# Performance work log

Measured on AMD Instinct MI355X. Metric: run time of the kernel, lower is better.

Reference implementation:

```python
import jax, jax.numpy as jnp
import numpy as np

D = 1024
M = 256
BATCH = 2048


def setup_inputs() -> dict:
    key = jax.random.key(0)
    kx, kw, kp = jax.random.split(key, 3)
    x = jax.random.uniform(kx, (BATCH, D), dtype=jnp.float32)
    W = jax.random.normal(kw, (M,), dtype=jnp.float32)
    P = jax.random.normal(kp, (M, D), dtype=jnp.float32)
    return {"x": x, "W": W, "P": P}


def reference(x, W, P):
    # log mixture weights: log softmax over m
    logw = jax.nn.log_softmax(W, axis=-1)              # [m]
    p = jax.nn.sigmoid(P)                              # [m, d]
    # broadcast Bernoulli likelihood: [batch, m, d]
    lik = x[:, None, :] * p[None, :, :] + (1.0 - x[:, None, :]) * (1.0 - p[None, :, :])
    # per-component log-likelihood summed over features, plus log weight
    comp_ll = jnp.sum(jnp.log(lik), axis=-1) + logw[None, :]   # [batch, m]
    # mixture log-likelihood via logsumexp over components
    return jax.scipy.special.logsumexp(comp_ll, axis=-1)       # [batch]
```

## Files before the change

### kernel.cpp

```cpp
#include <hip/hip_runtime.h>

#define BATCH 2048
#define MM    256
#define DD    1024

#define BB 128
#define BM 64
#define KC 16
#define TB 8
#define TM 4
#define LXS (BB + 4)
#define LRS (BM + 4)
#define NBT (BATCH / BB)

#define LOG2E 1.4426950408889634f
#define LN2   0.6931471805599453f

typedef float v2f __attribute__((ext_vector_type(2)));

__device__ __forceinline__ float fr_mant(float x) {
#if __has_builtin(__builtin_amdgcn_frexp_mantf)
    return __builtin_amdgcn_frexp_mantf(x);
#else
    unsigned u = __float_as_uint(x);
    return __uint_as_float((u & 0x807FFFFFu) | 0x3F000000u);
#endif
}
__device__ __forceinline__ int fr_exp(float x) {
#if __has_builtin(__builtin_amdgcn_frexp_expf)
    return __builtin_amdgcn_frexp_expf(x);
#else
    return (int)((__float_as_uint(x) >> 23) & 0xFFu) - 126;
#endif
}

__global__ __launch_bounds__(256) void precomp_kernel(
        const float* __restrict__ P, const float* __restrict__ Wv,
        float* __restrict__ rbuf, float* __restrict__ cst) {
    const int m = blockIdx.x;
    const int t = threadIdx.x;
    const int lane = t & 63, wid = t >> 6;

    float4 z = ((const float4*)(P + (size_t)m * DD))[t];
    float e0 = __expf(z.x), e1 = __expf(z.y), e2 = __expf(z.z), e3 = __expf(z.w);
    ((float4*)(rbuf + (size_t)m * DD))[t] =
        make_float4(e0 - 1.f, e1 - 1.f, e2 - 1.f, e3 - 1.f);
    float part = -(__log2f(1.f + e0) + __log2f(1.f + e1) +
                   __log2f(1.f + e2) + __log2f(1.f + e3));

    __shared__ float smA[4], smB[4];

    #pragma unroll
    for (int o = 32; o; o >>= 1) part += __shfl_xor(part, o);
    if (lane == 0) smA[wid] = part;

    float w = Wv[t];
    float mx = w;
    #pragma unroll
    for (int o = 32; o; o >>= 1) mx = fmaxf(mx, __shfl_xor(mx, o));
    if (lane == 0) smB[wid] = mx;
    __syncthreads();

    float rowc = smA[0] + smA[1] + smA[2] + smA[3];
    float gmx  = fmaxf(fmaxf(smB[0], smB[1]), fmaxf(smB[2], smB[3]));

    float se = __expf(w - gmx);
    #pragma unroll
    for (int o = 32; o; o >>= 1) se += __shfl_xor(se, o);
    __syncthreads();
    if (lane == 0) smA[wid] = se;
    __syncthreads();

    if (t == 0) {
        float sum = smA[0] + smA[1] + smA[2] + smA[3];
        cst[m] = rowc + (Wv[m] - gmx) * LOG2E - __log2f(sum);
    }
}

__global__ __launch_bounds__(256, 4) void main_kernel(
        const float* __restrict__ x, const float* __restrict__ rbuf,
        float* __restrict__ pbuf, int dc) {
    __shared__ __align__(16) float lx[KC * LXS];
    __shared__ __align__(16) float lr[KC * LRS];

    const int tid = threadIdx.x;
    const int tx = tid & 15;
    const int ty = tid >> 4;

    const int gid  = blockIdx.x;
    const int xcd  = gid & 7;
    const int k    = gid >> 3;
    const int m_id = k & 3;
    const int tile = (k >> 2) * 8 + xcd;
    const int b_id = tile & (NBT - 1);
    const int d_id = tile / NBT;

    const int m0 = m_id * BM;
    const int b0 = b_id * BB;
    const int d0 = d_id * dc;
    const int NC = dc / KC;

    const int rowx = tid >> 2, segx = tid & 3;
    const float* xp0 = x + (size_t)(b0 + rowx) * DD + d0 + segx * 4;
    const float* xp1 = xp0 + (size_t)64 * DD;
    const float* rp  = rbuf + (size_t)(m0 + rowx) * DD + d0 + segx * 4;

    float4 cx0 = *(const float4*)xp0;
    float4 cx1 = *(const float4*)xp1;
    float4 cr  = *(const float4*)rp;

    v2f prod2[TB / 2][TM];
    int acce[TB][TM];
    #pragma unroll
    for (int i2 = 0; i2 < TB / 2; ++i2)
        #pragma unroll
        for (int j = 0; j < TM; ++j) prod2[i2][j] = (v2f){1.0f, 1.0f};
    #pragma unroll
    for (int i = 0; i < TB; ++i)
        #pragma unroll
        for (int j = 0; j < TM; ++j) acce[i][j] = 0;

    const v2f one2 = (v2f){1.0f, 1.0f};

    for (int c = 0; c < NC; ++c) {
        __syncthreads();
        {
            const int base = segx * 4;
            lx[(base + 0) * LXS + rowx] = cx0.x;
            lx[(base + 1) * LXS + rowx] = cx0.y;
            lx[(base + 2) * LXS + rowx] = cx0.z;
            lx[(base + 3) * LXS + rowx] = cx0.w;
            lx[(base + 0) * LXS + rowx + 64] = cx1.x;
            lx[(base + 1) * LXS + rowx + 64] = cx1.y;
            lx[(base + 2) * LXS + rowx + 64] = cx1.z;
            lx[(base + 3) * LXS + rowx + 64] = cx1.w;
            if (rowx < BM) {
                lr[(base + 0) * LRS + rowx] = cr.x;
                lr[(base + 1) * LRS + rowx] = cr.y;
                lr[(base + 2) * LRS + rowx] = cr.z;
                lr[(base + 3) * LRS + rowx] = cr.w;
            }
        }
        if (c + 1 < NC) {
            xp0 += KC; xp1 += KC; rp += KC;
            cx0 = *(const float4*)xp0;
            cx1 = *(const float4*)xp1;
            cr  = *(const float4*)rp;
        }
        __syncthreads();

        #pragma unroll
        for (int kc = 0; kc < KC; ++kc) {
            const float4* xp = (const float4*)&lx[kc * LXS + TB * ty];
            float4 xa = xp[0], xb = xp[1];
            const float4* rpf = (const float4*)&lr[kc * LRS + TM * tx];
            float4 rv = rpf[0];
            v2f xs[TB / 2] = {(v2f){xa.x, xa.y}, (v2f){xa.z, xa.w},
                              (v2f){xb.x, xb.y}, (v2f){xb.z, xb.w}};
            v2f rs[TM] = {(v2f){rv.x, rv.x}, (v2f){rv.y, rv.y},
                          (v2f){rv.z, rv.z}, (v2f){rv.w, rv.w}};
            #pragma unroll
            for (int i2 = 0; i2 < TB / 2; ++i2)
                #pragma unroll
                for (int j = 0; j < TM; ++j) {
                    v2f t = __builtin_elementwise_fma(xs[i2], rs[j], one2);
                    prod2[i2][j] = prod2[i2][j] * t;
                }
        }
        #pragma unroll
        for (int i2 = 0; i2 < TB / 2; ++i2)
            #pragma unroll
            for (int j = 0; j < TM; ++j) {
                float p0 = prod2[i2][j].x, p1 = prod2[i2][j].y;
                acce[2 * i2 + 0][j] += fr_exp(p0);
                acce[2 * i2 + 1][j] += fr_exp(p1);
                prod2[i2][j] = (v2f){fr_mant(p0), fr_mant(p1)};
            }
    }

    float* pb = pbuf + ((size_t)d_id * BATCH + b0) * MM + m0;
    #pragma unroll
    for (int i = 0; i < TB; ++i) {
        const int i2 = i >> 1;
        float p0 = (i & 1) ? prod2[i2][0].y : prod2[i2][0].x;
        float p1 = (i & 1) ? prod2[i2][1].y : prod2[i2][1].x;
        float p2 = (i & 1) ? prod2[i2][2].y : prod2[i2][2].x;
        float p3 = (i & 1) ? prod2[i2][3].y : prod2[i2][3].x;
        float4 vv;
        vv.x = (float)acce[i][0] + __log2f(p0);
        vv.y = (float)acce[i][1] + __log2f(p1);
        vv.z = (float)acce[i][2] + __log2f(p2);
        vv.w = (float)acce[i][3] + __log2f(p3);
        *(float4*)&pb[(size_t)(TB * ty + i) * MM + TM * tx] = vv;
    }
}

__global__ __launch_bounds__(256) void finalize16_kernel(
        const float4* __restrict__ pbuf4, const float4* __restrict__ cst4,
        float* __restrict__ out) {
    const int lane = threadIdx.x & 63;
    const int w = threadIdx.x >> 6;
    const int b = blockIdx.x * 4 + w;

    float4 v = cst4[lane];
    const float4* pb = pbuf4 + (size_t)b * (MM / 4) + lane;
    #pragma unroll
    for (int s = 0; s < 16; ++s) {
        float4 t = pb[(size_t)s * BATCH * (MM / 4)];
        v.x += t.x; v.y += t.y; v.z += t.z; v.w += t.w;
    }

    float mx = fmaxf(fmaxf(v.x, v.y), fmaxf(v.z, v.w));
    #pragma unroll
    for (int o = 32; o; o >>= 1) mx = fmaxf(mx, __shfl_xor(mx, o));

    float s = exp2f(v.x - mx) + exp2f(v.y - mx) + exp2f(v.z - mx) + exp2f(v.w - mx);
    #pragma unroll
    for (int o = 32; o; o >>= 1) s += __shfl_xor(s, o);

    if (lane == 0) out[b] = LN2 * (mx + __log2f(s));
}

__global__ __launch_bounds__(256) void finalize_kernel(
        const float* __restrict__ pbuf, const float* __restrict__ cst,
        float* __restrict__ out, int sd) {
    const int lane = threadIdx.x & 63;
    const int w = threadIdx.x >> 6;
    const int b = blockIdx.x * 4 + w;

    float v0 = cst[lane];
    float v1 = cst[lane + 64];
    float v2 = cst[lane + 128];
    float v3 = cst[lane + 192];

    for (int s = 0; s < sd; ++s) {
        const float* row = pbuf + ((size_t)s * BATCH + b) * MM;
        v0 += row[lane];
        v1 += row[lane + 64];
        v2 += row[lane + 128];
        v3 += row[lane + 192];
    }

    float mx = fmaxf(fmaxf(v0, v1), fmaxf(v2, v3));
    #pragma unroll
    for (int o = 32; o; o >>= 1) mx = fmaxf(mx, __shfl_xor(mx, o));

    float s = exp2f(v0 - mx) + exp2f(v1 - mx) + exp2f(v2 - mx) + exp2f(v3 - mx);
    #pragma unroll
    for (int o = 32; o; o >>= 1) s += __shfl_xor(s, o);

    if (lane == 0) out[b] = LN2 * (mx + __log2f(s));
}

extern "C" void kernel_launch(void* const* d_in, const int* in_sizes, int n_in,
                              void* d_out, int out_size, void* d_ws, size_t ws_size,
                              hipStream_t stream) {
    const float* x  = (const float*)d_in[0];
    const float* Wv = (const float*)d_in[1];
    const float* P  = (const float*)d_in[2];

    float* ws   = (float*)d_ws;
    float* rbuf = ws;
    float* cst  = rbuf + (size_t)MM * DD;
    float* pbuf = cst + MM;

    size_t fixed = ((size_t)MM * DD + MM) * sizeof(float);
    size_t avail = (ws_size > fixed) ? (ws_size - fixed) : 0;
    int sd = 16;
    while (sd > 1 && (size_t)sd * BATCH * MM * sizeof(float) > avail) sd >>= 1;

    precomp_kernel<<<MM, 256, 0, stream>>>(P, Wv, rbuf, cst);
    int nblocks = NBT * sd * 4;
    main_kernel<<<nblocks, 256, 0, stream>>>(x, rbuf, pbuf, DD / sd);
    if (sd == 16)
        finalize16_kernel<<<BATCH / 4, 256, 0, stream>>>(
            (const float4*)pbuf, (const float4*)cst, (float*)d_out);
    else
        finalize_kernel<<<BATCH / 4, 256, 0, stream>>>(pbuf, cst, (float*)d_out, sd);
}
```

Measured before the change: 93.74 us.

## Enlarge main kernel tile to 128x128 with 8x8 per-thread register blocking

Doubles the component tile (BM 64→128) and per-thread component count (TM 4→8), so each thread computes an 8x8 block of products. The global-to-LDS load mapping is reworked so each thread loads two float4 per operand, and the column split is strided at 64 to avoid bank conflicts. The goal is fewer LDS reads and fewer redundant x loads per FMA. In exchange, register pressure roughly doubles, occupancy is lowered to 2 blocks per SIMD, and the grid has half as many blocks.

```diff
diff --git a/kernel.cpp b/kernel.cpp
--- a/kernel.cpp
+++ b/kernel.cpp
@@ -5,13 +5,14 @@
 #define DD    1024
 
 #define BB 128
-#define BM 64
+#define BM 128
 #define KC 16
 #define TB 8
-#define TM 4
+#define TM 8
 #define LXS (BB + 4)
 #define LRS (BM + 4)
 #define NBT (BATCH / BB)
+#define NMB (MM / BM)
 
 #define LOG2E 1.4426950408889634f
 #define LN2   0.6931471805599453f
@@ -77,7 +78,7 @@
     }
 }
 
-__global__ __launch_bounds__(256, 4) void main_kernel(
+__global__ __launch_bounds__(256, 2) void main_kernel(
         const float* __restrict__ x, const float* __restrict__ rbuf,
         float* __restrict__ pbuf, int dc) {
     __shared__ __align__(16) float lx[KC * LXS];
@@ -90,8 +91,8 @@
     const int gid  = blockIdx.x;
     const int xcd  = gid & 7;
     const int k    = gid >> 3;
-    const int m_id = k & 3;
-    const int tile = (k >> 2) * 8 + xcd;
+    const int m_id = k & (NMB - 1);
+    const int tile = (k >> 1) * 8 + xcd;
     const int b_id = tile & (NBT - 1);
     const int d_id = tile / NBT;
 
@@ -100,14 +101,14 @@
     const int d0 = d_id * dc;
     const int NC = dc / KC;
 
-    const int rowx = tid >> 2, segx = tid & 3;
-    const float* xp0 = x + (size_t)(b0 + rowx) * DD + d0 + segx * 4;
-    const float* xp1 = xp0 + (size_t)64 * DD;
-    const float* rp  = rbuf + (size_t)(m0 + rowx) * DD + d0 + segx * 4;
-
-    float4 cx0 = *(const float4*)xp0;
-    float4 cx1 = *(const float4*)xp1;
-    float4 cr  = *(const float4*)rp;
+    const int rowx = tid >> 1, segx = tid & 1;
+    const float* xp = x    + (size_t)(b0 + rowx) * DD + d0 + segx * 8;
+    const float* rp = rbuf + (size_t)(m0 + rowx) * DD + d0 + segx * 8;
+
+    float4 cx0 = ((const float4*)xp)[0];
+    float4 cx1 = ((const float4*)xp)[1];
+    float4 cr0 = ((const float4*)rp)[0];
+    float4 cr1 = ((const float4*)rp)[1];
 
     v2f prod2[TB / 2][TM];
     int acce[TB][TM];
@@ -125,45 +126,48 @@
     for (int c = 0; c < NC; ++c) {
         __syncthreads();
         {
-            const int base = segx * 4;
+            const int base = segx * 8;
             lx[(base + 0) * LXS + rowx] = cx0.x;
             lx[(base + 1) * LXS + rowx] = cx0.y;
             lx[(base + 2) * LXS + rowx] = cx0.z;
             lx[(base + 3) * LXS + rowx] = cx0.w;
-            lx[(base + 0) * LXS + rowx + 64] = cx1.x;
-            lx[(base + 1) * LXS + rowx + 64] = cx1.y;
-            lx[(base + 2) * LXS + rowx + 64] = cx1.z;
-            lx[(base + 3) * LXS + rowx + 64] = cx1.w;
-            if (rowx < BM) {
-                lr[(base + 0) * LRS + rowx] = cr.x;
-                lr[(base + 1) * LRS + rowx] = cr.y;
-                lr[(base + 2) * LRS + rowx] = cr.z;
-                lr[(base + 3) * LRS + rowx] = cr.w;
-            }
+            lx[(base + 4) * LXS + rowx] = cx1.x;
+            lx[(base + 5) * LXS + rowx] = cx1.y;
+            lx[(base + 6) * LXS + rowx] = cx1.z;
+            lx[(base + 7) * LXS + rowx] = cx1.w;
+            lr[(base + 0) * LRS + rowx] = cr0.x;
+            lr[(base + 1) * LRS + rowx] = cr0.y;
+            lr[(base + 2) * LRS + rowx] = cr0.z;
+            lr[(base + 3) * LRS + rowx] = cr0.w;
+            lr[(base + 4) * LRS + rowx] = cr1.x;
+            lr[(base + 5) * LRS + rowx] = cr1.y;
+            lr[(base + 6) * LRS + rowx] = cr1.z;
+            lr[(base + 7) * LRS + rowx] = cr1.w;
         }
         if (c + 1 < NC) {
-            xp0 += KC; xp1 += KC; rp += KC;
-            cx0 = *(const float4*)xp0;
-            cx1 = *(const float4*)xp1;
-            cr  = *(const float4*)rp;
+            xp += KC; rp += KC;
+            cx0 = ((const float4*)xp)[0];
+            cx1 = ((const float4*)xp)[1];
+            cr0 = ((const float4*)rp)[0];
+            cr1 = ((const float4*)rp)[1];
         }
         __syncthreads();
 
         #pragma unroll
         for (int kc = 0; kc < KC; ++kc) {
-            const float4* xp = (const float4*)&lx[kc * LXS + TB * ty];
-            float4 xa = xp[0], xb = xp[1];
-            const float4* rpf = (const float4*)&lr[kc * LRS + TM * tx];
-            float4 rv = rpf[0];
+            const float4* xpf = (const float4*)&lx[kc * LXS + TB * ty];
+            float4 xa = xpf[0], xb = xpf[1];
+            float4 ra = *(const float4*)&lr[kc * LRS + 4 * tx];
+            float4 rb = *(const float4*)&lr[kc * LRS + 64 + 4 * tx];
             v2f xs[TB / 2] = {(v2f){xa.x, xa.y}, (v2f){xa.z, xa.w},
                               (v2f){xb.x, xb.y}, (v2f){xb.z, xb.w}};
-            v2f rs[TM] = {(v2f){rv.x, rv.x}, (v2f){rv.y, rv.y},
-                          (v2f){rv.z, rv.z}, (v2f){rv.w, rv.w}};
+            float rf[TM] = {ra.x, ra.y, ra.z, ra.w, rb.x, rb.y, rb.z, rb.w};
             #pragma unroll
             for (int i2 = 0; i2 < TB / 2; ++i2)
                 #pragma unroll
                 for (int j = 0; j < TM; ++j) {
-                    v2f t = __builtin_elementwise_fma(xs[i2], rs[j], one2);
+                    v2f rs = (v2f){rf[j], rf[j]};
+                    v2f t = __builtin_elementwise_fma(xs[i2], rs, one2);
                     prod2[i2][j] = prod2[i2][j] * t;
                 }
         }
@@ -182,16 +186,18 @@
     #pragma unroll
     for (int i = 0; i < TB; ++i) {
         const int i2 = i >> 1;
-        float p0 = (i & 1) ? prod2[i2][0].y : prod2[i2][0].x;
-        float p1 = (i & 1) ? prod2[i2][1].y : prod2[i2][1].x;
-        float p2 = (i & 1) ? prod2[i2][2].y : prod2[i2][2].x;
-        float p3 = (i & 1) ? prod2[i2][3].y : prod2[i2][3].x;
-        float4 vv;
-        vv.x = (float)acce[i][0] + __log2f(p0);
-        vv.y = (float)acce[i][1] + __log2f(p1);
-        vv.z = (float)acce[i][2] + __log2f(p2);
-        vv.w = (float)acce[i][3] + __log2f(p3);
-        *(float4*)&pb[(size_t)(TB * ty + i) * MM + TM * tx] = vv;
+        float* row = pb + (size_t)(TB * ty + i) * MM;
+        float4 v0, v1;
+        v0.x = (float)acce[i][0] + __log2f((i & 1) ? prod2[i2][0].y : prod2[i2][0].x);
+        v0.y = (float)acce[i][1] + __log2f((i & 1) ? prod2[i2][1].y : prod2[i2][1].x);
+        v0.z = (float)acce[i][2] + __log2f((i & 1) ? prod2[i2][2].y : prod2[i2][2].x);
+        v0.w = (float)acce[i][3] + __log2f((i & 1) ? prod2[i2][3].y : prod2[i2][3].x);
+        v1.x = (float)acce[i][4] + __log2f((i & 1) ? prod2[i2][4].y : prod2[i2][4].x);
+        v1.y = (float)acce[i][5] + __log2f((i & 1) ? prod2[i2][5].y : prod2[i2][5].x);
+        v1.z = (float)acce[i][6] + __log2f((i & 1) ? prod2[i2][6].y : prod2[i2][6].x);
+        v1.w = (float)acce[i][7] + __log2f((i & 1) ? prod2[i2][7].y : prod2[i2][7].x);
+        *(float4*)&row[4 * tx]      = v0;
+        *(float4*)&row[64 + 4 * tx] = v1;
     }
 }
 
@@ -270,7 +276,7 @@
     while (sd > 1 && (size_t)sd * BATCH * MM * sizeof(float) > avail) sd >>= 1;
 
     precomp_kernel<<<MM, 256, 0, stream>>>(P, Wv, rbuf, cst);
-    int nblocks = NBT * sd * 4;
+    int nblocks = NBT * sd * NMB;
     main_kernel<<<nblocks, 256, 0, stream>>>(x, rbuf, pbuf, DD / sd);
     if (sd == 16)
         finalize16_kernel<<<BATCH / 4, 256, 0, stream>>>(
```

Measured after the change: 95.13 us. About the same (+1.5%).
